# Kernel optimization log

Measured on AMD Instinct MI355X. Metric: run time of the kernel, lower is better.

The kernel has to match this reference:

```python
import jax, jax.numpy as jnp
import numpy as np

N = 50000
E = 800000
EP = 200000
IN_C = 128
HID = 128


def setup_inputs() -> dict:
    key = jax.random.key(0)
    ks = jax.random.split(key, 10)
    x = jax.random.normal(ks[0], (N, IN_C), dtype=jnp.float32)
    edge_index = jax.random.randint(ks[1], (2, E), 0, N, dtype=jnp.int64)
    pred_edges = jax.random.randint(ks[2], (2, EP), 0, N, dtype=jnp.int64)
    s_in = 1.0 / np.sqrt(IN_C)
    s_h = 1.0 / np.sqrt(HID)
    W1l = jax.random.normal(ks[3], (IN_C, HID), dtype=jnp.float32) * s_in
    W1r = jax.random.normal(ks[4], (IN_C, HID), dtype=jnp.float32) * s_in
    b1 = jnp.zeros((HID,), dtype=jnp.float32)
    W2l = jax.random.normal(ks[5], (HID, HID), dtype=jnp.float32) * s_h
    W2r = jax.random.normal(ks[6], (HID, HID), dtype=jnp.float32) * s_h
    b2 = jnp.zeros((HID,), dtype=jnp.float32)
    return {"x": x, "W1l": W1l, "b1": b1, "W1r": W1r,
            "W2l": W2l, "b2": b2, "W2r": W2r,
            "edge_index": edge_index, "pred_edges": pred_edges}


def _sage_conv(h, Wl, b, Wr, src, dst, n_nodes):
    # PyG SAGEConv (aggr='mean'): out = lin_l(mean_j x_j) + lin_r(x_i)
    msg = h[src]                                              # (E, D) gather
    agg = jax.ops.segment_sum(msg, dst, num_segments=n_nodes)  # (N, D) scatter-add
    deg = jax.ops.segment_sum(jnp.ones((src.shape[0],), h.dtype), dst,
                              num_segments=n_nodes)
    agg = agg / jnp.maximum(deg, 1.0)[:, None]                # mean (0 for isolated)
    return agg @ Wl + b + h @ Wr


def reference(x, W1l, b1, W1r, W2l, b2, W2r, edge_index, pred_edges):
    n_nodes = x.shape[0]
    src, dst = edge_index[0], edge_index[1]
    h = jax.nn.relu(_sage_conv(x, W1l, b1, W1r, src, dst, n_nodes))
    z = _sage_conv(h, W2l, b2, W2r, src, dst, n_nodes)
    ps, pd = pred_edges[0], pred_edges[1]
    return jnp.sum(z[ps] * z[pd], axis=-1)  # (E_pred,) logits
```

## Files before the change

kernel.cpp:

```cpp
#include <hip/hip_runtime.h>

#define D 128

typedef __attribute__((ext_vector_type(8))) short short8;
typedef __attribute__((ext_vector_type(4))) float f32x4;

__device__ inline unsigned int f2bf_bits(float f) {
    unsigned int u = __float_as_uint(f);
    return (u + 0x7FFFu + ((u >> 16) & 1u)) >> 16;
}

__device__ inline float bfhi(unsigned int u) { return __uint_as_float(u << 16); }
__device__ inline float bflo(unsigned int u) { return __uint_as_float(u & 0xffff0000u); }

__global__ __launch_bounds__(256) void prep_kernel(
    const float* __restrict__ x,
    const float* __restrict__ W1l, const float* __restrict__ W1r,
    const float* __restrict__ W2l, const float* __restrict__ W2r,
    unsigned short* __restrict__ xbf, unsigned short* __restrict__ xlo,
    unsigned short* __restrict__ h1, unsigned short* __restrict__ l1,
    unsigned short* __restrict__ h2, unsigned short* __restrict__ l2,
    int n4, int ncast, int* __restrict__ chist, int* __restrict__ csrpad)
{
    const int b = blockIdx.x;
    const int t = threadIdx.x;
    if (b < ncast) {
        int i = b * 256 + t;
        if (i >= n4) return;
        f32x4 v = *(const f32x4*)(x + (size_t)i * 4);
        ushort4 oh, ol;
        {
            unsigned int h; float hf;
            h = f2bf_bits(v.x); hf = __uint_as_float(h << 16);
            oh.x = (unsigned short)h; ol.x = (unsigned short)f2bf_bits(v.x - hf);
            h = f2bf_bits(v.y); hf = __uint_as_float(h << 16);
            oh.y = (unsigned short)h; ol.y = (unsigned short)f2bf_bits(v.y - hf);
            h = f2bf_bits(v.z); hf = __uint_as_float(h << 16);
            oh.z = (unsigned short)h; ol.z = (unsigned short)f2bf_bits(v.z - hf);
            h = f2bf_bits(v.w); hf = __uint_as_float(h << 16);
            oh.w = (unsigned short)h; ol.w = (unsigned short)f2bf_bits(v.w - hf);
        }
        *(ushort4*)(xbf + (size_t)i * 4) = oh;
        *(ushort4*)(xlo + (size_t)i * 4) = ol;
    } else if (b < ncast + 256) {
        int gidx = (b - ncast) * 256 + t;
        int sel = gidx >> 15;
        int idx = gidx & 32767;
        int tt = idx >> 12;
        int ks = (idx >> 9) & 7;
        int lane = (idx >> 3) & 63;
        int j = idx & 7;
        int qq = lane >> 4, r16 = lane & 15;
        int k = ks * 32 + qq * 8 + j;
        int c = tt * 16 + r16;
        const float* Wl = sel ? W2l : W1l;
        const float* Wr = sel ? W2r : W1r;
        float v = (k < 128) ? Wl[k * 128 + c] : Wr[(k - 128) * 128 + c];
        unsigned int h = f2bf_bits(v);
        float hf = __uint_as_float(h << 16);
        unsigned int l = f2bf_bits(v - hf);
        (sel ? h2 : h1)[idx] = (unsigned short)h;
        (sel ? l2 : l1)[idx] = (unsigned short)l;
    } else {
        chist[t] = 0;
        if (t < 32) csrpad[t] = 0;
    }
}

__global__ __launch_bounds__(256) void coarse_count_kernel(const int* __restrict__ dst,
                                                           int* __restrict__ chist, int E) {
    __shared__ int h[256];
    h[threadIdx.x] = 0;
    __syncthreads();
    const int stride = gridDim.x * 256;
    for (int e = blockIdx.x * 256 + threadIdx.x; e < E; e += stride)
        atomicAdd(&h[dst[e] >> 8], 1);
    __syncthreads();
    int v = h[threadIdx.x];
    if (v) atomicAdd(&chist[threadIdx.x], v);
}

__global__ __launch_bounds__(256) void scan256_kernel(const int* __restrict__ chist,
                                                      int* __restrict__ cbase,
                                                      int* __restrict__ gcur) {
    __shared__ int wsum[4];
    const int t = threadIdx.x, lane = t & 63, wv = t >> 6;
    int v = chist[t];
    int s = v;
#pragma unroll
    for (int o = 1; o < 64; o <<= 1) {
        int u = __shfl_up(s, o, 64);
        if (lane >= o) s += u;
    }
    if (lane == 63) wsum[wv] = s;
    __syncthreads();
    int add = 0;
    for (int w = 0; w < wv; ++w) add += wsum[w];
    cbase[t + 1] = s + add;
    if (t == 0) cbase[0] = 0;
    gcur[t] = s + add - v;
}

#define CCHUNK 4096
__global__ __launch_bounds__(256) void coarse_scatter_kernel(
    const int* __restrict__ src, const int* __restrict__ dst,
    int* __restrict__ gcur, unsigned int* __restrict__ centries, int E)
{
    __shared__ int h[256];
    __shared__ int base[256];
    __shared__ unsigned int stage[CCHUNK];
    const int t = threadIdx.x;
    const int e0 = blockIdx.x * CCHUNK;
    h[t] = 0;
    __syncthreads();
#pragma unroll
    for (int i = 0; i < 16; ++i) {
        int e = e0 + i * 256 + t;
        unsigned int u = 0xFFFFFFFFu;
        if (e < E) {
            int d = dst[e];
            int s = src[e];
            int b = d >> 8;
            u = ((unsigned)b << 24) | ((unsigned)s << 8) | (unsigned)(d & 255);
            atomicAdd(&h[b], 1);
        }
        stage[i * 256 + t] = u;
    }
    __syncthreads();
    base[t] = atomicAdd(&gcur[t], h[t]);
    __syncthreads();
    h[t] = 0;
    __syncthreads();
#pragma unroll
    for (int i = 0; i < 16; ++i) {
        unsigned int u = stage[i * 256 + t];
        if (u != 0xFFFFFFFFu) {
            int b = u >> 24;
            int r = atomicAdd(&h[b], 1);
            centries[base[b] + r] = u & 0x00FFFFFFu;
        }
    }
}

#define DCAP 8192
__global__ __launch_bounds__(256) void fine_bucket_kernel(
    const unsigned int* __restrict__ centries,
    const int* __restrict__ cbase,
    int* __restrict__ offo, int* __restrict__ csr, int N, int E)
{
    __shared__ int h[256], ex[256], wsum[4];
    __shared__ int stg[DCAP];
    const int t = threadIdx.x, lane = t & 63, wv = t >> 6;
    const int b = blockIdx.x;
    const int s0 = cbase[b];
    const int cnt = cbase[b + 1] - s0;
    h[t] = 0;
    __syncthreads();
    for (int i = t; i < cnt; i += 256)
        atomicAdd(&h[centries[s0 + i] & 255], 1);
    __syncthreads();
    int v = h[t], s = v;
#pragma unroll
    for (int o = 1; o < 64; o <<= 1) {
        int u = __shfl_up(s, o, 64);
        if (lane >= o) s += u;
    }
    if (lane == 63) wsum[wv] = s;
    __syncthreads();
    int add = 0;
    for (int w = 0; w < wv; ++w) add += wsum[w];
    const int exc = s + add - v;
    ex[t] = exc;
    const int dg = b * 256 + t;
    if (dg < N) offo[dg] = s0 + exc;
    if (b == 0 && t == 0) offo[N] = E;
    h[t] = 0;
    __syncthreads();
    if (cnt <= DCAP) {
        for (int i = t; i < cnt; i += 256) {
            unsigned int u = centries[s0 + i];
            int dl = u & 255;
            int r = atomicAdd(&h[dl], 1);
            stg[ex[dl] + r] = (int)(u >> 8);
        }
        __syncthreads();
        for (int i = t; i < cnt; i += 256)
            csr[s0 + i] = stg[i];
    } else {
        for (int i = t; i < cnt; i += 256) {
            unsigned int u = centries[s0 + i];
            int dl = u & 255;
            int r = atomicAdd(&h[dl], 1);
            csr[s0 + ex[dl] + r] = (int)(u >> 8);
        }
    }
}

__global__ __launch_bounds__(256, 4) void fused_sage_kernel(
    const unsigned short* __restrict__ featbf,
    const int* __restrict__ off,
    const int* __restrict__ csr,
    const unsigned short* __restrict__ self_hi,
    const unsigned short* __restrict__ self_lo,
    const unsigned short* __restrict__ wpk_hi,
    const unsigned short* __restrict__ wpk_lo,
    const float* __restrict__ bias,
    unsigned short* __restrict__ out_hi,
    unsigned short* __restrict__ out_lo,
    int do_relu)
{
    __shared__ unsigned short AHs[4][64][8];
    __shared__ unsigned short ALs[4][64][8];
    __shared__ unsigned short outs_hi[16][128];
    __shared__ unsigned short outs_lo[16][128];

    const int w = threadIdx.x >> 6;
    const int l = threadIdx.x & 63;
    const int tile = blockIdx.x;
    const int n0w = tile * 16;

    const int gn = l >> 2;
    const int q2 = l & 3;
    const int gnode = n0w + gn;
    const int start = off[gnode];
    const int end   = off[gnode + 1];
    const unsigned short* fb = featbf + w * 32 + q2 * 8;

    float ga[8] = {0.f, 0.f, 0.f, 0.f, 0.f, 0.f, 0.f, 0.f};

#define LDIX(dst, be)                                             \
    { int4 tt_ = *(const int4*)(csr + (be));                      \
      dst.x = ((be)     < end) ? tt_.x : 0;                       \
      dst.y = ((be) + 1 < end) ? tt_.y : 0;                       \
      dst.z = ((be) + 2 < end) ? tt_.z : 0;                       \
      dst.w = ((be) + 3 < end) ? tt_.w : 0; }

#define LDROWS(ix, r0, r1, r2, r3)                                \
    r0 = *(const uint4*)(fb + (size_t)(ix).x * D);                \
    r1 = *(const uint4*)(fb + (size_t)(ix).y * D);                \
    r2 = *(const uint4*)(fb + (size_t)(ix).z * D);                \
    r3 = *(const uint4*)(fb + (size_t)(ix).w * D);

#define ACCP(r, o)                                                       \
    { uint4 rv = r;                                                      \
      if (e + (o) >= end) { rv.x = 0u; rv.y = 0u; rv.z = 0u; rv.w = 0u; }\
      ga[0] += bfhi(rv.x); ga[1] += bflo(rv.x);                          \
      ga[2] += bfhi(rv.y); ga[3] += bflo(rv.y);                          \
      ga[4] += bfhi(rv.z); ga[5] += bflo(rv.z);                          \
      ga[6] += bfhi(rv.w); ga[7] += bflo(rv.w); }

    if (start < end) {
        int4 ixA, ixB;
        uint4 a0, a1, a2, a3, b0, b1, b2, b3;
        LDIX(ixA, start);
        LDROWS(ixA, a0, a1, a2, a3)
        LDIX(ixB, start + 4);
        int e = start;
        for (;;) {
            LDROWS(ixB, b0, b1, b2, b3)
            LDIX(ixA, e + 8);
            __builtin_amdgcn_sched_barrier(0);
            ACCP(a0, 0) ACCP(a1, 1) ACCP(a2, 2) ACCP(a3, 3)
            e += 4;
            if (e >= end) break;
            LDROWS(ixA, a0, a1, a2, a3)
            LDIX(ixB, e + 8);
            __builtin_amdgcn_sched_barrier(0);
            ACCP(b0, 0) ACCP(b1, 1) ACCP(b2, 2) ACCP(b3, 3)
            e += 4;
            if (e >= end) break;
        }
    }
#undef ACCP
#undef LDROWS
#undef LDIX

    {
        const float dinv = 1.0f / (float)max(end - start, 1);
        short8 hi8, lo8;
#pragma unroll
        for (int c = 0; c < 8; ++c) {
            float v = ga[c] * dinv;
            unsigned int hb = f2bf_bits(v);
            hi8[c] = (short)hb;
            lo8[c] = (short)f2bf_bits(v - __uint_as_float(hb << 16));
        }
        *(short8*)&AHs[w][q2 * 16 + gn][0] = hi8;
        *(short8*)&ALs[w][q2 * 16 + gn][0] = lo8;
    }
    __syncthreads();

    const int q = l >> 4, r16 = l & 15;
    const int mnode = n0w + r16;
    f32x4 acc0 = {0.f, 0.f, 0.f, 0.f};
    f32x4 acc1 = {0.f, 0.f, 0.f, 0.f};
    const unsigned short* sph = self_hi + (size_t)mnode * D + q * 8;
    const unsigned short* spl = self_lo + (size_t)mnode * D + q * 8;
    const unsigned short* bh0 = wpk_hi + (size_t)(2 * w) * 4096 + l * 8;
    const unsigned short* bl0 = wpk_lo + (size_t)(2 * w) * 4096 + l * 8;

#pragma unroll
    for (int ks = 0; ks < 8; ++ks) {
        short8 AH, AL;
        if (ks < 4) {
            AH = *(const short8*)&AHs[ks][l][0];
            AL = *(const short8*)&ALs[ks][l][0];
        } else {
            AH = *(const short8*)(sph + (ks - 4) * 32);
            AL = *(const short8*)(spl + (ks - 4) * 32);
        }
        short8 BH0 = *(const short8*)(bh0 + ks * 512);
        short8 BL0 = *(const short8*)(bl0 + ks * 512);
        short8 BH1 = *(const short8*)(bh0 + 4096 + ks * 512);
        short8 BL1 = *(const short8*)(bl0 + 4096 + ks * 512);
        acc0 = __builtin_amdgcn_mfma_f32_16x16x32_bf16(AH, BH0, acc0, 0, 0, 0);
        acc0 = __builtin_amdgcn_mfma_f32_16x16x32_bf16(AL, BH0, acc0, 0, 0, 0);
        acc0 = __builtin_amdgcn_mfma_f32_16x16x32_bf16(AH, BL0, acc0, 0, 0, 0);
        acc1 = __builtin_amdgcn_mfma_f32_16x16x32_bf16(AH, BH1, acc1, 0, 0, 0);
        acc1 = __builtin_amdgcn_mfma_f32_16x16x32_bf16(AL, BH1, acc1, 0, 0, 0);
        acc1 = __builtin_amdgcn_mfma_f32_16x16x32_bf16(AH, BL1, acc1, 0, 0, 0);
    }

    {
        const float bv0 = bias[32 * w + r16];
        const float bv1 = bias[32 * w + 16 + r16];
#pragma unroll
        for (int r = 0; r < 4; ++r) {
            float v0 = acc0[r] + bv0;
            float v1 = acc1[r] + bv1;
            if (do_relu) { v0 = fmaxf(v0, 0.f); v1 = fmaxf(v1, 0.f); }
            const int row = q * 4 + r;
            unsigned int h0 = f2bf_bits(v0);
            unsigned int h1 = f2bf_bits(v1);
            outs_hi[row][32 * w + r16] = (unsigned short)h0;
            outs_hi[row][32 * w + 16 + r16] = (unsigned short)h1;
            outs_lo[row][32 * w + r16] =
                (unsigned short)f2bf_bits(v0 - __uint_as_float(h0 << 16));
            outs_lo[row][32 * w + 16 + r16] =
                (unsigned short)f2bf_bits(v1 - __uint_as_float(h1 << 16));
        }
    }
    __syncthreads();
    {
        const int tid = threadIdx.x;
        short8 vh = *(short8*)(&outs_hi[0][0] + tid * 8);
        *(short8*)(out_hi + (size_t)n0w * D + tid * 8) = vh;
        if (out_lo) {
            short8 vl = *(short8*)(&outs_lo[0][0] + tid * 8);
            *(short8*)(out_lo + (size_t)n0w * D + tid * 8) = vl;
        }
    }
}

__global__ __launch_bounds__(256) void pred_kernel(const unsigned short* __restrict__ zbf,
                                                   const int* __restrict__ ps,
                                                   const int* __restrict__ pd,
                                                   float* __restrict__ out, int EP) {
    int idx = blockIdx.x * 256 + threadIdx.x;
    int e = idx >> 4;
    if (e >= EP) return;
    int L = idx & 15;
    const unsigned short* fb = zbf + (size_t)L * 8;
    uint4 ra = *(const uint4*)(fb + (size_t)ps[e] * D);
    uint4 rb = *(const uint4*)(fb + (size_t)pd[e] * D);
    float p = bfhi(ra.x) * bfhi(rb.x) + bflo(ra.x) * bflo(rb.x)
            + bfhi(ra.y) * bfhi(rb.y) + bflo(ra.y) * bflo(rb.y)
            + bfhi(ra.z) * bfhi(rb.z) + bflo(ra.z) * bflo(rb.z)
            + bfhi(ra.w) * bfhi(rb.w) + bflo(ra.w) * bflo(rb.w);
#pragma unroll
    for (int off = 8; off > 0; off >>= 1) p += __shfl_xor(p, off, 16);
    if (L == 0) out[e] = p;
}

extern "C" void kernel_launch(void* const* d_in, const int* in_sizes, int n_in,
                              void* d_out, int out_size, void* d_ws, size_t ws_size,
                              hipStream_t stream) {
    const float* x   = (const float*)d_in[0];
    const float* W1l = (const float*)d_in[1];
    const float* b1  = (const float*)d_in[2];
    const float* W1r = (const float*)d_in[3];
    const float* W2l = (const float*)d_in[4];
    const float* b2  = (const float*)d_in[5];
    const float* W2r = (const float*)d_in[6];
    const int* edge_index = (const int*)d_in[7];
    const int* pred_edges = (const int*)d_in[8];
    float* out = (float*)d_out;

    const int N  = in_sizes[0] / D;
    const int E  = in_sizes[7] / 2;
    const int EP = in_sizes[8] / 2;

    const int* src = edge_index;
    const int* dst = edge_index + E;
    const int* ps  = pred_edges;
    const int* pd  = pred_edges + EP;

    int* chist   = (int*)d_ws;
    int* cbase   = chist + 256;
    int* gcur    = cbase + 272;
    int* off     = gcur + 256;
    unsigned int* centries = (unsigned int*)(off + 50016);
    int* csr     = (int*)(centries + E);
    unsigned short* w1_hi = (unsigned short*)(csr + E + 32);
    unsigned short* w1_lo = w1_hi + 32768;
    unsigned short* w2_hi = w1_lo + 32768;
    unsigned short* w2_lo = w2_hi + 32768;
    unsigned short* xbf   = w2_lo + 32768;
    unsigned short* xlo   = xbf + (size_t)N * D;
    unsigned short* hbf   = xlo + (size_t)N * D;
    unsigned short* hlo   = hbf + (size_t)N * D;
    unsigned short* zbf   = hlo + (size_t)N * D;

    const int n4 = N * D / 4;
    const int ncast = (n4 + 255) / 256;
    const int ntiles = N / 16;
    const int nbC = (E + CCHUNK - 1) / CCHUNK;
    const int nbD = (N + 255) / 256;
    const int nblk_pred = (EP * 16 + 255) / 256;

    prep_kernel<<<ncast + 257, 256, 0, stream>>>(x, W1l, W1r, W2l, W2r,
                                                 xbf, xlo, w1_hi, w1_lo, w2_hi, w2_lo,
                                                 n4, ncast, chist, csr + E);

    coarse_count_kernel<<<256, 256, 0, stream>>>(dst, chist, E);
    scan256_kernel<<<1, 256, 0, stream>>>(chist, cbase, gcur);
    coarse_scatter_kernel<<<nbC, 256, 0, stream>>>(src, dst, gcur, centries, E);
    fine_bucket_kernel<<<nbD, 256, 0, stream>>>(centries, cbase, off, csr, N, E);

    fused_sage_kernel<<<ntiles, 256, 0, stream>>>(xbf, off, csr, xbf, xlo,
                                                  w1_hi, w1_lo, b1, hbf, hlo, 1);
    fused_sage_kernel<<<ntiles, 256, 0, stream>>>(hbf, off, csr, hbf, hlo,
                                                  w2_hi, w2_lo, b2, zbf,
                                                  (unsigned short*)nullptr, 0);
    pred_kernel<<<nblk_pred, 256, 0, stream>>>(zbf, ps, pd, out, EP);
}
```

Baseline: 248.0 us.

## Stream neighbor rows into LDS via async global_load_lds double buffering

Replaces the register-staged gather of neighbor feature rows with asynchronous global-to-LDS loads (global_load_lds, 16 bytes per lane) into a per-wave double buffer. A manual s_waitcnt vmcnt lets the next batch of four rows stream in while the current batch is accumulated from LDS. The aim is to free the VGPRs that held in-flight rows and keep more loads outstanding. In exchange, LDS use grows to 40KB per block, which could limit occupancy, and correctness relies on the hand-written vmcnt count matching the outstanding loads.

```diff
diff --git a/kernel.cpp b/kernel.cpp
--- a/kernel.cpp
+++ b/kernel.cpp
@@ -12,6 +12,12 @@
 
 __device__ inline float bfhi(unsigned int u) { return __uint_as_float(u << 16); }
 __device__ inline float bflo(unsigned int u) { return __uint_as_float(u & 0xffff0000u); }
+
+__device__ inline void gld16(const void* g, void* l) {
+    __builtin_amdgcn_global_load_lds(
+        (const __attribute__((address_space(1))) void*)g,
+        (__attribute__((address_space(3))) void*)l, 16, 0, 0);
+}
 
 __global__ __launch_bounds__(256) void prep_kernel(
     const float* __restrict__ x,
@@ -209,15 +215,17 @@
     unsigned short* __restrict__ out_lo,
     int do_relu)
 {
-    __shared__ unsigned short AHs[4][64][8];
-    __shared__ unsigned short ALs[4][64][8];
-    __shared__ unsigned short outs_hi[16][128];
-    __shared__ unsigned short outs_lo[16][128];
+    __shared__ __align__(16) unsigned char smem[40960];
+    unsigned short (*AHs)[64][8] = (unsigned short (*)[64][8])(smem + 32768);
+    unsigned short (*ALs)[64][8] = (unsigned short (*)[64][8])(smem + 36864);
+    unsigned short (*outs_hi)[128] = (unsigned short (*)[128])(smem);
+    unsigned short (*outs_lo)[128] = (unsigned short (*)[128])(smem + 4096);
 
     const int w = threadIdx.x >> 6;
     const int l = threadIdx.x & 63;
     const int tile = blockIdx.x;
     const int n0w = tile * 16;
+    unsigned char* stw = smem + w * 8192;
 
     const int gn = l >> 2;
     const int q2 = l & 3;
@@ -229,50 +237,45 @@
     float ga[8] = {0.f, 0.f, 0.f, 0.f, 0.f, 0.f, 0.f, 0.f};
 
 #define LDIX(dst, be)                                             \
-    { int4 tt_ = *(const int4*)(csr + (be));                      \
-      dst.x = ((be)     < end) ? tt_.x : 0;                       \
-      dst.y = ((be) + 1 < end) ? tt_.y : 0;                       \
-      dst.z = ((be) + 2 < end) ? tt_.z : 0;                       \
-      dst.w = ((be) + 3 < end) ? tt_.w : 0; }
-
-#define LDROWS(ix, r0, r1, r2, r3)                                \
-    r0 = *(const uint4*)(fb + (size_t)(ix).x * D);                \
-    r1 = *(const uint4*)(fb + (size_t)(ix).y * D);                \
-    r2 = *(const uint4*)(fb + (size_t)(ix).z * D);                \
-    r3 = *(const uint4*)(fb + (size_t)(ix).w * D);
-
-#define ACCP(r, o)                                                       \
-    { uint4 rv = r;                                                      \
-      if (e + (o) >= end) { rv.x = 0u; rv.y = 0u; rv.z = 0u; rv.w = 0u; }\
+    { int4 t_ = *(const int4*)(csr + (be));                       \
+      dst.x = ((be)     < end) ? t_.x : 0;                        \
+      dst.y = ((be) + 1 < end) ? t_.y : 0;                        \
+      dst.z = ((be) + 2 < end) ? t_.z : 0;                        \
+      dst.w = ((be) + 3 < end) ? t_.w : 0; }
+
+#define GLD4(sbase, ix)                                           \
+    gld16(fb + (size_t)(ix).x * D, (sbase));                      \
+    gld16(fb + (size_t)(ix).y * D, (sbase) + 1024);               \
+    gld16(fb + (size_t)(ix).z * D, (sbase) + 2048);               \
+    gld16(fb + (size_t)(ix).w * D, (sbase) + 3072);
+
+#define ACCL(k)                                                          \
+    { uint4 rv = *(const uint4*)(stw + cur * 4096 + (k) * 1024 + l * 16);\
+      if (e + (k) >= end) { rv.x = 0u; rv.y = 0u; rv.z = 0u; rv.w = 0u; }\
       ga[0] += bfhi(rv.x); ga[1] += bflo(rv.x);                          \
       ga[2] += bfhi(rv.y); ga[3] += bflo(rv.y);                          \
       ga[4] += bfhi(rv.z); ga[5] += bflo(rv.z);                          \
       ga[6] += bfhi(rv.w); ga[7] += bflo(rv.w); }
 
     if (start < end) {
-        int4 ixA, ixB;
-        uint4 a0, a1, a2, a3, b0, b1, b2, b3;
-        LDIX(ixA, start);
-        LDROWS(ixA, a0, a1, a2, a3)
-        LDIX(ixB, start + 4);
-        int e = start;
+        int4 ix0, ixn, ixf;
+        LDIX(ix0, start);
+        LDIX(ixn, start + 4);
+        GLD4(stw, ix0)
+        int e = start, cur = 0;
         for (;;) {
-            LDROWS(ixB, b0, b1, b2, b3)
-            LDIX(ixA, e + 8);
-            __builtin_amdgcn_sched_barrier(0);
-            ACCP(a0, 0) ACCP(a1, 1) ACCP(a2, 2) ACCP(a3, 3)
+            LDIX(ixf, e + 8);
+            GLD4(stw + (cur ^ 1) * 4096, ixn)
+            asm volatile("s_waitcnt vmcnt(5)" ::: "memory");
+            ACCL(0) ACCL(1) ACCL(2) ACCL(3)
             e += 4;
             if (e >= end) break;
-            LDROWS(ixA, a0, a1, a2, a3)
-            LDIX(ixB, e + 8);
-            __builtin_amdgcn_sched_barrier(0);
-            ACCP(b0, 0) ACCP(b1, 1) ACCP(b2, 2) ACCP(b3, 3)
-            e += 4;
-            if (e >= end) break;
-        }
-    }
-#undef ACCP
-#undef LDROWS
+            cur ^= 1;
+            ixn = ixf;
+        }
+    }
+#undef ACCL
+#undef GLD4
 #undef LDIX
 
     {
```

Measured after the change: 256.0 us. 1.03x slower.
